# Kernel tuning notes

Measured on AMD Instinct MI355X. Metric: run time of the kernel, lower is better.

Reference implementation:

```python
import jax, jax.numpy as jnp
import numpy as np

D_MODEL = 1024
H = 16
D_K = D_MODEL // H
B = 4
S = 2048


def setup_inputs() -> dict:
    key = jax.random.key(0)
    ks = jax.random.split(key, 7)
    q = jax.random.normal(ks[0], (B, S, D_MODEL), dtype=jnp.float32)
    k = jax.random.normal(ks[1], (B, S, D_MODEL), dtype=jnp.float32)
    v = jax.random.normal(ks[2], (B, S, D_MODEL), dtype=jnp.float32)
    # nn.Linear weights have shape (out_features, in_features); y = x @ W.T
    scale = 1.0 / np.sqrt(D_MODEL)
    w_q = jax.random.normal(ks[3], (D_MODEL, D_MODEL), dtype=jnp.float32) * scale
    w_k = jax.random.normal(ks[4], (D_MODEL, D_MODEL), dtype=jnp.float32) * scale
    w_v = jax.random.normal(ks[5], (D_MODEL, D_MODEL), dtype=jnp.float32) * scale
    w_o = jax.random.normal(ks[6], (D_MODEL, D_MODEL), dtype=jnp.float32) * scale
    mask = jnp.ones((1, 1, S, S), dtype=bool)  # broadcasts over [B,H,S,S]
    return {"q": q, "k": k, "v": v, "w_q": w_q, "w_k": w_k, "w_v": w_v,
            "w_o": w_o, "mask": mask}


def reference(q, k, v, w_q, w_k, w_v, w_o, mask):
    # projections (nn.Linear, no bias): x @ W.T
    query = jnp.einsum('bsd,ed->bse', q, w_q)
    key_p = jnp.einsum('bsd,ed->bse', k, w_k)
    value = jnp.einsum('bsd,ed->bse', v, w_v)
    # split heads: [B,S,D] -> [B,H,S,d_k]
    query = query.reshape(B, S, H, D_K).transpose(0, 2, 1, 3)
    key_p = key_p.reshape(B, S, H, D_K).transpose(0, 2, 1, 3)
    value = value.reshape(B, S, H, D_K).transpose(0, 2, 1, 3)
    # scaled dot-product attention (explicit softmax, as in source)
    scores = jnp.einsum('bhqd,bhkd->bhqk', query, key_p) / jnp.sqrt(
        jnp.asarray(D_K, dtype=query.dtype))
    scores = jnp.where(mask, scores, jnp.asarray(-1e9, dtype=scores.dtype))
    weights = jax.nn.softmax(scores, axis=-1)
    ctx = jnp.einsum('bhqk,bhkd->bhqd', weights, value)
    # merge heads and output projection
    ctx = ctx.transpose(0, 2, 1, 3).reshape(B, S, D_MODEL)
    return jnp.einsum('bsd,ed->bse', ctx, w_o)
```

## Files before the change

### kernel.cpp

```cpp
#include <hip/hip_runtime.h>
#include <hip/hip_bf16.h>
#include <stdint.h>
#include <math.h>

#define DM 1024
#define SS 2048
#define HH 16

typedef unsigned short u16;
typedef __attribute__((ext_vector_type(8))) short short8;
typedef __attribute__((ext_vector_type(4))) float f32x4;
typedef __attribute__((ext_vector_type(4))) unsigned short u16x4;

#define C_SCALE 0.18033688011112042f

__device__ __forceinline__ u16 f2bf(float f) {
    union { float f; uint32_t u; } v; v.f = f;
    uint32_t r = v.u + 0x7FFFu + ((v.u >> 16) & 1u);
    return (u16)(r >> 16);
}

__device__ __forceinline__ void async_cp16(const void* g, void* l) {
    __builtin_amdgcn_global_load_lds(
        reinterpret_cast<const __attribute__((address_space(1))) unsigned int*>(
            reinterpret_cast<uintptr_t>(g)),
        reinterpret_cast<__attribute__((address_space(3))) unsigned int*>(
            reinterpret_cast<uintptr_t>(l)),
        16, 0, 0);
}

__device__ __forceinline__ short8 pack8(const float4 a, const float4 b) {
    union { short8 s; struct { __hip_bfloat162 p0, p1, p2, p3; } p; } u;
    u.p.p0 = __float22bfloat162_rn(make_float2(a.x, a.y));
    u.p.p1 = __float22bfloat162_rn(make_float2(a.z, a.w));
    u.p.p2 = __float22bfloat162_rn(make_float2(b.x, b.y));
    u.p.p3 = __float22bfloat162_rn(make_float2(b.z, b.w));
    return u.s;
}

__global__ __launch_bounds__(256) void cast_w4(const float* __restrict__ w0,
                                               const float* __restrict__ w1,
                                               const float* __restrict__ w2,
                                               const float* __restrict__ w3,
                                               u16* __restrict__ o0,
                                               u16* __restrict__ o1,
                                               u16* __restrict__ o2,
                                               u16* __restrict__ o3)
{
    const uint32_t which = blockIdx.x >> 10;
    const uint32_t i = (blockIdx.x & 1023u) * 256u + threadIdx.x;
    const float* in = which == 0 ? w0 : which == 1 ? w1 : which == 2 ? w2 : w3;
    u16* out = which == 0 ? o0 : which == 1 ? o1 : which == 2 ? o2 : o3;
    float4 v = ((const float4*)in)[i];
    u16x4 p = { f2bf(v.x), f2bf(v.y), f2bf(v.z), f2bf(v.w) };
    ((u16x4*)out)[i] = p;
}

__global__ __launch_bounds__(256) void gemm_castA3(const float* __restrict__ Aq,
                                                   const float* __restrict__ Ak,
                                                   const float* __restrict__ Av,
                                                   const u16* __restrict__ Bq,
                                                   const u16* __restrict__ Bk,
                                                   const u16* __restrict__ Bv,
                                                   u16* __restrict__ Cq,
                                                   u16* __restrict__ Ck,
                                                   u16* __restrict__ Cv)
{
    __shared__ char sm[49152];
    const uint32_t t = threadIdx.x;
    const uint32_t l = t & 63u, w = t >> 6;
    const uint32_t sw = (blockIdx.x & 7u) * 192u + (blockIdx.x >> 3);
    const uint32_t which = sw >> 9;
    const uint32_t inner = sw & 511u;
    const uint32_t bm = inner >> 3, bn = inner & 7u;
    const uint32_t wr = w >> 1, wc = w & 1u;

    const float* A = which == 0 ? Aq : which == 1 ? Ak : Av;
    const u16*   B = which == 0 ? Bq : which == 1 ? Bk : Bv;

    const uint32_t q15 = l & 15u, G = l >> 4, xq = q15 & 7u;
    const uint32_t vA0  = wr * 16384u + q15 * 256u + ((2u * G ^ xq) << 4);
    const uint32_t vA0x = vA0 ^ 16u;
    const uint32_t vbg0 = q15 * 128u + ((G ^ (xq & 3u)) << 4) + ((xq >> 2) << 6);
    const uint32_t vB0 = 32768u + wc * 8192u + vbg0, vB1 = vB0 ^ 64u;

    uint32_t LA[8];
    const float* aP[8];
    #pragma unroll
    for (uint32_t i = 0; i < 8; ++i) {
        const uint32_t j = i * 256u + t, row = j >> 4, ch = j & 15u;
        const uint32_t c8 = ch ^ (row & 7u);
        aP[i] = A + (size_t)(bm * 128u + row) * DM + c8 * 4u;
        LA[i] = j * 16u;
    }
    uint32_t LB[4];
    const u16* bP[4];
    #pragma unroll
    for (uint32_t i = 0; i < 4; ++i) {
        LB[i] = (i * 256u + t) * 16u;
        const uint32_t r = LB[i] >> 7;
        const uint32_t c8 = ((LB[i] >> 4) & 7u) ^ (r & 7u);
        bP[i] = B + (size_t)(bn * 128u + r) * DM + c8 * 8u;
    }

    f32x4 acc[4][4] = {};

    for (uint32_t k0 = 0; k0 < 1024; k0 += 64) {
        __syncthreads();
        #pragma unroll
        for (uint32_t i = 0; i < 8; ++i) async_cp16(aP[i] + k0, sm + LA[i]);
        #pragma unroll
        for (uint32_t i = 0; i < 4; ++i) async_cp16(bP[i] + k0, sm + 32768 + LB[i]);
        __syncthreads();

        #pragma unroll
        for (uint32_t kk = 0; kk < 2; ++kk) {
            const uint32_t ao = kk * 128u;
            const uint32_t vb = kk ? vB1 : vB0;
            short8 a[4], bfr[4];
            #pragma unroll
            for (uint32_t m = 0; m < 4; ++m) {
                float4 lo = *(const float4*)(sm + vA0  + ao + m * 4096u);
                float4 hi = *(const float4*)(sm + vA0x + ao + m * 4096u);
                a[m] = pack8(lo, hi);
            }
            #pragma unroll
            for (uint32_t n = 0; n < 4; ++n)
                bfr[n] = *(const short8*)(sm + vb + n * 2048u);
            #pragma unroll
            for (uint32_t m = 0; m < 4; ++m)
                #pragma unroll
                for (uint32_t n = 0; n < 4; ++n)
                    acc[m][n] = __builtin_amdgcn_mfma_f32_16x16x32_bf16(
                        a[m], bfr[n], acc[m][n], 0, 0, 0);
        }
    }

    u16* Cb = which == 0 ? Cq : which == 1 ? Ck : Cv;
    const float sc = which == 0 ? C_SCALE : 1.0f;
    #pragma unroll
    for (uint32_t m = 0; m < 4; ++m) {
        #pragma unroll
        for (uint32_t n = 0; n < 4; ++n) {
            const uint32_t rmb = bm * 128u + wr * 64u + m * 16u + G * 4u;
            const uint32_t cn  = bn * 128u + wc * 64u + n * 16u + q15;
            if (which != 2) {
                #pragma unroll
                for (uint32_t g = 0; g < 4; ++g)
                    Cb[(size_t)(rmb + g) * DM + cn] = f2bf(acc[m][n][g] * sc);
            } else {
                const uint32_t b_ = rmb >> 11, s0 = rmb & 2047u;
                u16x4 pk;
                #pragma unroll
                for (uint32_t g = 0; g < 4; ++g) pk[g] = f2bf(acc[m][n][g]);
                *(u16x4*)(Cb + (size_t)(b_ * 1024u + cn) * 2048u + s0) = pk;
            }
        }
    }
}

__global__ __launch_bounds__(256) void gemm_out(const u16* __restrict__ A,
                                                const u16* __restrict__ B,
                                                float* __restrict__ C)
{
    __shared__ char sm[32768];
    const uint32_t t = threadIdx.x;
    const uint32_t l = t & 63u, w = t >> 6;
    uint32_t id = blockIdx.x;
    id = (id & 7u) * 64u + (id >> 3);
    const uint32_t bm = id >> 3, bn = id & 7u;
    const uint32_t wr = w >> 1, wc = w & 1u;

    const uint32_t q15 = l & 15u, G = l >> 4, xq = q15 & 7u;
    const uint32_t vbg0 = q15 * 128u + ((G ^ (xq & 3u)) << 4) + ((xq >> 2) << 6);
    const uint32_t vA0 = wr * 8192u + vbg0,          vA1 = vA0 ^ 64u;
    const uint32_t vB0 = 16384u + wc * 8192u + vbg0, vB1 = vB0 ^ 64u;

    uint32_t La[4];
    const u16* aP[4];
    const u16* bP[4];
    #pragma unroll
    for (uint32_t i = 0; i < 4; ++i) {
        La[i] = (i * 256u + t) * 16u;
        const uint32_t r = La[i] >> 7;
        const uint32_t c8 = ((La[i] >> 4) & 7u) ^ (r & 7u);
        aP[i] = A + (size_t)(bm * 128u + r) * DM + c8 * 8u;
        bP[i] = B + (size_t)(bn * 128u + r) * DM + c8 * 8u;
    }

    f32x4 acc[4][4] = {};

    for (uint32_t k0 = 0; k0 < 1024; k0 += 64) {
        __syncthreads();
        #pragma unroll
        for (uint32_t i = 0; i < 4; ++i) async_cp16(aP[i] + k0, sm + La[i]);
        #pragma unroll
        for (uint32_t i = 0; i < 4; ++i) async_cp16(bP[i] + k0, sm + 16384 + La[i]);
        __syncthreads();

        #pragma unroll
        for (uint32_t kk = 0; kk < 2; ++kk) {
            const uint32_t va = kk ? vA1 : vA0;
            const uint32_t vb = kk ? vB1 : vB0;
            short8 a[4], b[4];
            #pragma unroll
            for (uint32_t m = 0; m < 4; ++m)
                a[m] = *(const short8*)(sm + va + m * 2048u);
            #pragma unroll
            for (uint32_t n = 0; n < 4; ++n)
                b[n] = *(const short8*)(sm + vb + n * 2048u);
            #pragma unroll
            for (uint32_t m = 0; m < 4; ++m)
                #pragma unroll
                for (uint32_t n = 0; n < 4; ++n)
                    acc[m][n] = __builtin_amdgcn_mfma_f32_16x16x32_bf16(
                        a[m], b[n], acc[m][n], 0, 0, 0);
        }
    }

    #pragma unroll
    for (uint32_t m = 0; m < 4; ++m) {
        #pragma unroll
        for (uint32_t n = 0; n < 4; ++n) {
            const uint32_t rmb = bm * 128u + wr * 64u + m * 16u + G * 4u;
            const uint32_t cn  = bn * 128u + wc * 64u + n * 16u + q15;
            #pragma unroll
            for (uint32_t g = 0; g < 4; ++g)
                C[(size_t)(rmb + g) * DM + cn] = acc[m][n][g];
        }
    }
}

__global__ __launch_bounds__(512) void attn_mfma(const u16* __restrict__ Q,
                                                 const u16* __restrict__ K,
                                                 const u16* __restrict__ Vt,
                                                 u16* __restrict__ ctx)
{
    __shared__ char sm[69632];
    const uint32_t t = threadIdx.x, l = t & 63u, w = t >> 6;
    uint32_t id = blockIdx.x;
    id = (id & 7u) * 64u + (id >> 3);
    const uint32_t qt = id & 7u, h = (id >> 3) & 15u, b = id >> 7;

    const uint32_t q15 = l & 15u, G = l >> 4, xq = q15 & 7u;

    const uint32_t vb0 = q15 * 128u + ((G ^ (xq & 3u)) << 4) + ((xq >> 2) << 6);
    const uint32_t vb1 = vb0 ^ 64u;
    const uint32_t vbPw = w * 4608u + q15 * 144u + G * 8u;
    const uint32_t vbPr = w * 4608u + q15 * 144u + G * 16u;

    short8 qf[2][2];
    #pragma unroll
    for (uint32_t qb = 0; qb < 2; ++qb) {
        const size_t qrow = (size_t)(b * 2048u + qt * 256u + w * 32u + qb * 16u + q15);
        const uint32_t col = h * 64u + (G << 3);
        qf[qb][0] = *(const short8*)(Q + qrow * DM + col);
        qf[qb][1] = *(const short8*)(Q + qrow * DM + col + 32u);
    }

    short8 ones;
    #pragma unroll
    for (int i = 0; i < 8; ++i) ones[i] = (short)0x3F80;
    const f32x4 ZV = {0.f, 0.f, 0.f, 0.f};

    f32x4 o[2][4] = {};
    f32x4 osum[2] = {};

    const uint32_t Ls = t * 16u;
    const u16* kcur;
    const u16* vcur;
    {
        const size_t kbase = (size_t)b * 2048u * DM + h * 64u;
        const size_t vbase = (size_t)((b * 16u + h) * 64u) * 2048u;
        const uint32_t r = Ls >> 7;
        const uint32_t c8 = ((Ls >> 4) & 7u) ^ (r & 7u);
        const u16* k0p = K  + kbase + (size_t)r * DM    + c8 * 8u;
        const u16* v0p = Vt + vbase + (size_t)r * 2048u + c8 * 8u;
        async_cp16(k0p, sm + Ls);
        async_cp16(v0p, sm + 8192 + Ls);
        kcur = k0p + (size_t)64u * DM;
        vcur = v0p + 64u;
    }

#define ATTN_STEP(BCc, BNc, STAGE)                                             \
    {                                                                          \
        if (STAGE) {                                                           \
            async_cp16(kcur, sm + (BNc) + Ls);                                 \
            async_cp16(vcur, sm + (BNc) + 8192u + Ls);                         \
            kcur += (size_t)64u * DM;                                          \
            vcur += 64u;                                                       \
            asm volatile("s_waitcnt vmcnt(2)" ::: "memory");                   \
        } else {                                                               \
            asm volatile("s_waitcnt vmcnt(0)" ::: "memory");                   \
        }                                                                      \
        __builtin_amdgcn_s_barrier();                                          \
        __builtin_amdgcn_sched_barrier(0);                                     \
        f32x4 s[2][4];                                                         \
        __builtin_amdgcn_s_setprio(1);                                         \
        _Pragma("unroll")                                                      \
        for (uint32_t mf = 0; mf < 4; ++mf) {                                  \
            short8 kf0 = *(const short8*)(sm + (BCc) + vb0 + mf * 2048u);      \
            short8 kf1 = *(const short8*)(sm + (BCc) + vb1 + mf * 2048u);      \
            _Pragma("unroll")                                                  \
            for (uint32_t qb = 0; qb < 2; ++qb) {                              \
                s[qb][mf] = __builtin_amdgcn_mfma_f32_16x16x32_bf16(           \
                    kf1, qf[qb][1],                                            \
                    __builtin_amdgcn_mfma_f32_16x16x32_bf16(                   \
                        kf0, qf[qb][0], ZV, 0, 0, 0),                          \
                    0, 0, 0);                                                  \
            }                                                                  \
        }                                                                      \
        __builtin_amdgcn_s_setprio(0);                                         \
        _Pragma("unroll")                                                      \
        for (uint32_t qb = 0; qb < 2; ++qb) {                                  \
            _Pragma("unroll")                                                  \
            for (uint32_t mf = 0; mf < 4; ++mf) {                              \
                float p0 = __builtin_amdgcn_exp2f(s[qb][mf][0]);               \
                float p1 = __builtin_amdgcn_exp2f(s[qb][mf][1]);               \
                float p2 = __builtin_amdgcn_exp2f(s[qb][mf][2]);               \
                float p3 = __builtin_amdgcn_exp2f(s[qb][mf][3]);               \
                union { u16x4 v; struct { __hip_bfloat162 lo, hi; } b; } pk;   \
                pk.b.lo = __float22bfloat162_rn(make_float2(p0, p1));          \
                pk.b.hi = __float22bfloat162_rn(make_float2(p2, p3));          \
                *(u16x4*)(sm + 32768u + vbPw + qb * 2304u + mf * 32u) = pk.v;  \
            }                                                                  \
        }                                                                      \
        _Pragma("unroll")                                                      \
        for (uint32_t kk = 0; kk < 2; ++kk) {                                  \
            const uint32_t vv = (kk ? vb1 : vb0) + 8192u;                      \
            short8 vf[4];                                                      \
            _Pragma("unroll")                                                  \
            for (uint32_t d = 0; d < 4; ++d)                                   \
                vf[d] = *(const short8*)(sm + (BCc) + vv + d * 2048u);         \
            __builtin_amdgcn_s_setprio(1);                                     \
            _Pragma("unroll")                                                  \
            for (uint32_t qb = 0; qb < 2; ++qb) {                              \
                short8 pf = *(const short8*)(sm + 32768u + vbPr +              \
                                             qb * 2304u + kk * 64u);           \
                _Pragma("unroll")                                              \
                for (uint32_t d = 0; d < 4; ++d)                               \
                    o[qb][d] = __builtin_amdgcn_mfma_f32_16x16x32_bf16(        \
                        pf, vf[d], o[qb][d], 0, 0, 0);                         \
                osum[qb] = __builtin_amdgcn_mfma_f32_16x16x32_bf16(            \
                    pf, ones, osum[qb], 0, 0, 0);                              \
            }                                                                  \
            __builtin_amdgcn_s_setprio(0);                                     \
        }                                                                      \
        asm volatile("s_waitcnt lgkmcnt(0)" ::: "memory");                     \
        __builtin_amdgcn_s_barrier();                                          \
        __builtin_amdgcn_sched_barrier(0);                                     \
    }

    for (uint32_t it = 0; it < 15; ++it) {
        ATTN_STEP(0u, 16384u, true)
        ATTN_STEP(16384u, 0u, true)
    }
    ATTN_STEP(0u, 16384u, true)
    ATTN_STEP(16384u, 0u, false)

#undef ATTN_STEP

    #pragma unroll
    for (uint32_t qb = 0; qb < 2; ++qb) {
        float inv[4];
        #pragma unroll
        for (int g = 0; g < 4; ++g) inv[g] = 1.0f / osum[qb][g];
        #pragma unroll
        for (uint32_t d = 0; d < 4; ++d)
            #pragma unroll
            for (int g = 0; g < 4; ++g) {
                const uint32_t srow = qt * 256u + w * 32u + qb * 16u + G * 4u + (uint32_t)g;
                const uint32_t col  = h * 64u + d * 16u + q15;
                ctx[(size_t)(b * 2048u + srow) * DM + col] = f2bf(o[qb][d][g] * inv[g]);
            }
    }
}

extern "C" void kernel_launch(void* const* d_in, const int* in_sizes, int n_in,
                              void* d_out, int out_size, void* d_ws, size_t ws_size,
                              hipStream_t stream)
{
    const float* q  = (const float*)d_in[0];
    const float* k  = (const float*)d_in[1];
    const float* v  = (const float*)d_in[2];
    const float* wq = (const float*)d_in[3];
    const float* wk = (const float*)d_in[4];
    const float* wv = (const float*)d_in[5];
    const float* wo = (const float*)d_in[6];

    const size_t SZ = (size_t)4 * 2048 * 1024;
    const size_t WZ = (size_t)1024 * 1024;
    u16* ctx = (u16*)d_ws;
    u16* Qp  = ctx + SZ;
    u16* Kp  = Qp  + SZ;
    u16* Vtp = Kp  + SZ;
    u16* wqb = Vtp + SZ;
    u16* wkb = wqb + WZ;
    u16* wvb = wkb + WZ;
    u16* wob = wvb + WZ;

    cast_w4<<<4096, 256, 0, stream>>>(wq, wk, wv, wo, wqb, wkb, wvb, wob);

    gemm_castA3<<<1536, 256, 0, stream>>>(q, k, v, wqb, wkb, wvb, Qp, Kp, Vtp);

    attn_mfma<<<512, 512, 0, stream>>>(Qp, Kp, Vtp, ctx);

    gemm_out<<<512, 256, 0, stream>>>(ctx, wob, (float*)d_out);
}
```

Baseline: 180.6 us.

## Triple-buffer K/V tiles and drop per-step trailing barrier in attention loop

Moves the attention K/V staging from double to triple buffering, with two tiles prefetched up front and the next load issued after compute. This lets each step use a single barrier instead of two. The P scratch buffer is also shrunk to one qb slice per warp, reused across qb iterations, which lowers LDS use. Only one barrier now separates a buffer's reads from its refill and the P reuse across qb, so correctness depends on careful wait counts.

```diff
diff --git a/kernel.cpp b/kernel.cpp
--- a/kernel.cpp
+++ b/kernel.cpp
@@ -236,7 +236,7 @@
                                                  const u16* __restrict__ Vt,
                                                  u16* __restrict__ ctx)
 {
-    __shared__ char sm[69632];
+    __shared__ char sm[67584];
     const uint32_t t = threadIdx.x, l = t & 63u, w = t >> 6;
     uint32_t id = blockIdx.x;
     id = (id & 7u) * 64u + (id >> 3);
@@ -246,8 +246,8 @@
 
     const uint32_t vb0 = q15 * 128u + ((G ^ (xq & 3u)) << 4) + ((xq >> 2) << 6);
     const uint32_t vb1 = vb0 ^ 64u;
-    const uint32_t vbPw = w * 4608u + q15 * 144u + G * 8u;
-    const uint32_t vbPr = w * 4608u + q15 * 144u + G * 16u;
+    const uint32_t vbPw = w * 2304u + q15 * 144u + G * 8u;
+    const uint32_t vbPr = w * 2304u + q15 * 144u + G * 16u;
 
     short8 qf[2][2];
     #pragma unroll
@@ -278,29 +278,23 @@
         const u16* v0p = Vt + vbase + (size_t)r * 2048u + c8 * 8u;
         async_cp16(k0p, sm + Ls);
         async_cp16(v0p, sm + 8192 + Ls);
-        kcur = k0p + (size_t)64u * DM;
-        vcur = v0p + 64u;
-    }
-
-#define ATTN_STEP(BCc, BNc, STAGE)                                             \
+        async_cp16(k0p + (size_t)64u * DM, sm + 16384 + Ls);
+        async_cp16(v0p + 64u, sm + 16384 + 8192 + Ls);
+        kcur = k0p + (size_t)128u * DM;
+        vcur = v0p + 128u;
+    }
+    asm volatile("s_waitcnt vmcnt(2)" ::: "memory");
+
+#define ATTN_STEP(CURB, STGB, MODE)                                            \
     {                                                                          \
-        if (STAGE) {                                                           \
-            async_cp16(kcur, sm + (BNc) + Ls);                                 \
-            async_cp16(vcur, sm + (BNc) + 8192u + Ls);                         \
-            kcur += (size_t)64u * DM;                                          \
-            vcur += 64u;                                                       \
-            asm volatile("s_waitcnt vmcnt(2)" ::: "memory");                   \
-        } else {                                                               \
-            asm volatile("s_waitcnt vmcnt(0)" ::: "memory");                   \
-        }                                                                      \
         __builtin_amdgcn_s_barrier();                                          \
         __builtin_amdgcn_sched_barrier(0);                                     \
         f32x4 s[2][4];                                                         \
         __builtin_amdgcn_s_setprio(1);                                         \
         _Pragma("unroll")                                                      \
         for (uint32_t mf = 0; mf < 4; ++mf) {                                  \
-            short8 kf0 = *(const short8*)(sm + (BCc) + vb0 + mf * 2048u);      \
-            short8 kf1 = *(const short8*)(sm + (BCc) + vb1 + mf * 2048u);      \
+            short8 kf0 = *(const short8*)(sm + (CURB) + vb0 + mf * 2048u);     \
+            short8 kf1 = *(const short8*)(sm + (CURB) + vb1 + mf * 2048u);     \
             _Pragma("unroll")                                                  \
             for (uint32_t qb = 0; qb < 2; ++qb) {                              \
                 s[qb][mf] = __builtin_amdgcn_mfma_f32_16x16x32_bf16(           \
@@ -322,41 +316,46 @@
                 union { u16x4 v; struct { __hip_bfloat162 lo, hi; } b; } pk;   \
                 pk.b.lo = __float22bfloat162_rn(make_float2(p0, p1));          \
                 pk.b.hi = __float22bfloat162_rn(make_float2(p2, p3));          \
-                *(u16x4*)(sm + 32768u + vbPw + qb * 2304u + mf * 32u) = pk.v;  \
+                *(u16x4*)(sm + 49152u + vbPw + mf * 32u) = pk.v;               \
             }                                                                  \
-        }                                                                      \
-        _Pragma("unroll")                                                      \
-        for (uint32_t kk = 0; kk < 2; ++kk) {                                  \
-            const uint32_t vv = (kk ? vb1 : vb0) + 8192u;                      \
-            short8 vf[4];                                                      \
             _Pragma("unroll")                                                  \
-            for (uint32_t d = 0; d < 4; ++d)                                   \
-                vf[d] = *(const short8*)(sm + (BCc) + vv + d * 2048u);         \
-            __builtin_amdgcn_s_setprio(1);                                     \
-            _Pragma("unroll")                                                  \
-            for (uint32_t qb = 0; qb < 2; ++qb) {                              \
-                short8 pf = *(const short8*)(sm + 32768u + vbPr +              \
-                                             qb * 2304u + kk * 64u);           \
+            for (uint32_t kk = 0; kk < 2; ++kk) {                              \
+                const uint32_t vv = (kk ? vb1 : vb0) + 8192u;                  \
+                short8 vf[4];                                                  \
+                _Pragma("unroll")                                              \
+                for (uint32_t d = 0; d < 4; ++d)                               \
+                    vf[d] = *(const short8*)(sm + (CURB) + vv + d * 2048u);    \
+                short8 pf = *(const short8*)(sm + 49152u + vbPr + kk * 64u);   \
+                __builtin_amdgcn_s_setprio(1);                                 \
                 _Pragma("unroll")                                              \
                 for (uint32_t d = 0; d < 4; ++d)                               \
                     o[qb][d] = __builtin_amdgcn_mfma_f32_16x16x32_bf16(        \
                         pf, vf[d], o[qb][d], 0, 0, 0);                         \
                 osum[qb] = __builtin_amdgcn_mfma_f32_16x16x32_bf16(            \
                     pf, ones, osum[qb], 0, 0, 0);                              \
+                __builtin_amdgcn_s_setprio(0);                                 \
             }                                                                  \
-            __builtin_amdgcn_s_setprio(0);                                     \
+            asm volatile("s_waitcnt lgkmcnt(0)" ::: "memory");                 \
         }                                                                      \
-        asm volatile("s_waitcnt lgkmcnt(0)" ::: "memory");                     \
-        __builtin_amdgcn_s_barrier();                                          \
+        if ((MODE) == 0) {                                                     \
+            async_cp16(kcur, sm + (STGB) + Ls);                                \
+            async_cp16(vcur, sm + (STGB) + 8192u + Ls);                        \
+            kcur += (size_t)64u * DM;                                          \
+            vcur += 64u;                                                       \
+            asm volatile("s_waitcnt vmcnt(2)" ::: "memory");                   \
+        } else if ((MODE) == 1) {                                              \
+            asm volatile("s_waitcnt vmcnt(0)" ::: "memory");                   \
+        }                                                                      \
         __builtin_amdgcn_sched_barrier(0);                                     \
     }
 
-    for (uint32_t it = 0; it < 15; ++it) {
-        ATTN_STEP(0u, 16384u, true)
-        ATTN_STEP(16384u, 0u, true)
-    }
-    ATTN_STEP(0u, 16384u, true)
-    ATTN_STEP(16384u, 0u, false)
+    for (uint32_t it = 0; it < 10; ++it) {
+        ATTN_STEP(0u,     32768u, 0)
+        ATTN_STEP(16384u, 0u,     0)
+        ATTN_STEP(32768u, 16384u, 0)
+    }
+    ATTN_STEP(0u,     0u, 1)
+    ATTN_STEP(16384u, 0u, 2)
 
 #undef ATTN_STEP
 
```

Measured after the change: 183.3 us. No clear change (+1.5%).

## Double-buffer LDS tiles in output projection GEMM with async prefetch

Applied to the files above, without the earlier changes.

The output projection GEMM now uses two 32KB LDS buffers and prefetches the next K-tile with async global-to-LDS copies while the current tile is consumed by MFMAs. Manual vmcnt waits and raw barriers replace the two __syncthreads per iteration, and setprio raises wave priority around the MFMA block. This is meant to hide global load latency in one of several kernels, at the cost of doubling LDS per block, which may lower occupancy.

```diff
diff --git a/kernel.cpp b/kernel.cpp
--- a/kernel.cpp
+++ b/kernel.cpp
@@ -163,7 +163,7 @@
                                                 const u16* __restrict__ B,
                                                 float* __restrict__ C)
 {
-    __shared__ char sm[32768];
+    __shared__ char sm[65536];
     const uint32_t t = threadIdx.x;
     const uint32_t l = t & 63u, w = t >> 6;
     uint32_t id = blockIdx.x;
@@ -190,33 +190,59 @@
 
     f32x4 acc[4][4] = {};
 
-    for (uint32_t k0 = 0; k0 < 1024; k0 += 64) {
-        __syncthreads();
-        #pragma unroll
-        for (uint32_t i = 0; i < 4; ++i) async_cp16(aP[i] + k0, sm + La[i]);
-        #pragma unroll
-        for (uint32_t i = 0; i < 4; ++i) async_cp16(bP[i] + k0, sm + 16384 + La[i]);
-        __syncthreads();
-
-        #pragma unroll
-        for (uint32_t kk = 0; kk < 2; ++kk) {
-            const uint32_t va = kk ? vA1 : vA0;
-            const uint32_t vb = kk ? vB1 : vB0;
-            short8 a[4], b[4];
-            #pragma unroll
-            for (uint32_t m = 0; m < 4; ++m)
-                a[m] = *(const short8*)(sm + va + m * 2048u);
-            #pragma unroll
-            for (uint32_t n = 0; n < 4; ++n)
-                b[n] = *(const short8*)(sm + vb + n * 2048u);
-            #pragma unroll
-            for (uint32_t m = 0; m < 4; ++m)
-                #pragma unroll
-                for (uint32_t n = 0; n < 4; ++n)
-                    acc[m][n] = __builtin_amdgcn_mfma_f32_16x16x32_bf16(
-                        a[m], b[n], acc[m][n], 0, 0, 0);
-        }
-    }
+    #pragma unroll
+    for (uint32_t i = 0; i < 4; ++i) async_cp16(aP[i], sm + La[i]);
+    #pragma unroll
+    for (uint32_t i = 0; i < 4; ++i) async_cp16(bP[i], sm + 16384 + La[i]);
+
+#define GEMM_STEP(CURB, STGB, STG, MODE)                                       \
+    {                                                                          \
+        if ((MODE) == 0) {                                                     \
+            _Pragma("unroll")                                                  \
+            for (uint32_t i = 0; i < 4; ++i)                                   \
+                async_cp16(aP[i] + (STG), sm + (STGB) + La[i]);                \
+            _Pragma("unroll")                                                  \
+            for (uint32_t i = 0; i < 4; ++i)                                   \
+                async_cp16(bP[i] + (STG), sm + (STGB) + 16384u + La[i]);       \
+            asm volatile("s_waitcnt vmcnt(8)" ::: "memory");                   \
+        } else {                                                               \
+            asm volatile("s_waitcnt vmcnt(0)" ::: "memory");                   \
+        }                                                                      \
+        __builtin_amdgcn_s_barrier();                                          \
+        __builtin_amdgcn_sched_barrier(0);                                     \
+        _Pragma("unroll")                                                      \
+        for (uint32_t kk = 0; kk < 2; ++kk) {                                  \
+            const uint32_t va = (CURB) + (kk ? vA1 : vA0);                     \
+            const uint32_t vb = (CURB) + (kk ? vB1 : vB0);                     \
+            short8 a[4], b[4];                                                 \
+            _Pragma("unroll")                                                  \
+            for (uint32_t m = 0; m < 4; ++m)                                   \
+                a[m] = *(const short8*)(sm + va + m * 2048u);                  \
+            _Pragma("unroll")                                                  \
+            for (uint32_t n = 0; n < 4; ++n)                                   \
+                b[n] = *(const short8*)(sm + vb + n * 2048u);                  \
+            __builtin_amdgcn_s_setprio(1);                                     \
+            _Pragma("unroll")                                                  \
+            for (uint32_t m = 0; m < 4; ++m)                                   \
+                _Pragma("unroll")                                              \
+                for (uint32_t n = 0; n < 4; ++n)                               \
+                    acc[m][n] = __builtin_amdgcn_mfma_f32_16x16x32_bf16(       \
+                        a[m], b[n], acc[m][n], 0, 0, 0);                       \
+            __builtin_amdgcn_s_setprio(0);                                     \
+        }                                                                      \
+        asm volatile("s_waitcnt lgkmcnt(0)" ::: "memory");                     \
+        __builtin_amdgcn_s_barrier();                                          \
+        __builtin_amdgcn_sched_barrier(0);                                     \
+    }
+
+    for (uint32_t it = 0; it < 7; ++it) {
+        GEMM_STEP(0u,     32768u, it * 128u + 64u,  0)
+        GEMM_STEP(32768u, 0u,     it * 128u + 128u, 0)
+    }
+    GEMM_STEP(0u,     32768u, 960u, 0)
+    GEMM_STEP(32768u, 0u,     0u,   1)
+
+#undef GEMM_STEP
 
     #pragma unroll
     for (uint32_t m = 0; m < 4; ++m) {
```

Measured after the change: 178.2 us (median of 2 runs). About the same (-1.3%).
